# Kernel optimization log

Hardware: AMD Instinct MI355X
Metric: run time of the kernel (lower is better)

The kernel has to match this reference:

```python
import jax, jax.numpy as jnp
import numpy as np

N_NODE = 200000   # item catalog size (n_node)
EMB = 100         # emb_size
NNZ = 1000000     # hypergraph adjacency nonzeros
B = 1024          # batch / cl_size
L = 50            # session length
LAYERS = 2        # HyperConv layers (opt.layer)
TAU = 0.2         # contrastive temperature
K_NEI = 3         # FindNeighbors.neighbor_n


def setup_inputs() -> dict:
    key = jax.random.key(0)
    ks = jax.random.split(key, 16)
    g = 1.414 / np.sqrt(EMB)  # xavier_normal gain=1.414 scale
    inp = {}
    inp["embedding"] = jax.random.normal(ks[0], (N_NODE, EMB), jnp.float32) * 0.1
    inp["adj_val"] = jax.random.uniform(ks[1], (NNZ,), jnp.float32)
    inp["A"] = jax.random.uniform(ks[2], (B, B), jnp.float32) * 0.01
    inp["D"] = jax.random.uniform(ks[3], (B, B), jnp.float32) * 0.01
    inp["z2"] = jax.random.normal(ks[4], (B, EMB), jnp.float32)
    inp["Wcf1"] = jax.random.normal(ks[5], (EMB, EMB), jnp.float32) * g
    inp["bcf1"] = jnp.zeros((EMB,), jnp.float32)
    inp["Wcf2"] = jax.random.normal(ks[6], (EMB, EMB), jnp.float32) * g
    inp["bcf2"] = jnp.zeros((EMB,), jnp.float32)
    inp["Wkg1"] = jax.random.normal(ks[7], (EMB, EMB), jnp.float32) * g
    inp["bkg1"] = jnp.zeros((EMB,), jnp.float32)
    inp["Wkg2"] = jax.random.normal(ks[8], (EMB, EMB), jnp.float32) * g
    inp["bkg2"] = jnp.zeros((EMB,), jnp.float32)
    inp["session_len"] = jnp.full((B, 1), float(L), jnp.float32)
    inp["adj_row"] = jax.random.randint(ks[9], (NNZ,), 0, N_NODE, jnp.int32)
    inp["adj_col"] = jax.random.randint(ks[10], (NNZ,), 0, N_NODE, jnp.int32)
    inp["items"] = jax.random.randint(ks[11], (B, L), 0, N_NODE + 1, jnp.int32)
    return inp


def _proj(z, W1, b1, W2, b2):
    # nn.Linear -> ELU -> nn.Linear (Contrast_2view projector)
    return jax.nn.elu(z @ W1.T + b1) @ W2.T + b2


def reference(embedding, adj_val, A, D, z2,
              Wcf1, bcf1, Wcf2, bcf2, Wkg1, bkg1, Wkg2, bkg2,
              session_len, adj_row, adj_col, items):
    # ---- HyperConv: layered sparse propagation, averaged over layers ----
    h = embedding
    acc = embedding
    for _ in range(LAYERS):
        # torch.sparse.mm(adjacency, h) via gather + segment_sum
        h = jax.ops.segment_sum(adj_val[:, None] * h[adj_col], adj_row,
                                num_segments=N_NODE)
        acc = acc + h
    hyper = acc / (LAYERS + 1)  # [N_NODE, EMB]

    # ---- RelationGAT.forward ----
    emb_pad = jnp.concatenate([jnp.zeros((1, EMB), hyper.dtype), hyper], axis=0)
    seq_h = emb_pad[items]                       # [B, L, EMB]
    rel = jnp.sum(seq_h, axis=1) / session_len   # [B, EMB]
    rel = (D @ A) @ rel                          # session-graph conv
    c = jax.nn.selu(rel)
    l_c = c / jnp.linalg.norm(c, axis=-1, keepdims=True)  # [B, EMB]

    # ---- FindNeighbors (dropout omitted: eval mode) ----
    sess = l_c
    norms = jnp.sqrt(jnp.sum(sess * sess + 1e-6, axis=1, keepdims=True))
    cos = (sess @ sess.T) / (norms @ norms.T)    # [B, B]
    cos = jax.nn.softmax(cos, axis=-1)
    topv, topi = jax.lax.top_k(cos, K_NEI)       # [B, K]
    topv = jax.nn.softmax(topv, axis=-1)
    neighbor = jnp.sum(topv[:, :, None] * sess[topi], axis=1)  # [B, EMB]

    # ---- Contrast_2view ----
    z1p = _proj(sess, Wcf1, bcf1, Wcf2, bcf2)
    z2p = _proj(z2, Wkg1, bkg1, Wkg2, bkg2)
    n1 = jnp.linalg.norm(z1p, axis=-1, keepdims=True)
    n2 = jnp.linalg.norm(z2p, axis=-1, keepdims=True)
    simm = jnp.exp((z1p @ z2p.T) / (n1 @ n2.T) / TAU)
    simm = simm / (jnp.sum(simm, axis=1, keepdims=True) + 1e-8)
    cl_loss = -jnp.mean(jnp.log(jnp.diagonal(simm)))  # pos = eye

    return hyper, l_c, neighbor, cl_loss
```

## Files before the change

### kernel.cpp

```cpp
#include <hip/hip_runtime.h>
#include <hip/hip_bf16.h>

#define N_NODE 200000
#define EMB 100
#define NNZ 1000000
#define BATCH 1024
#define SLEN 50
#define BE (BATCH * EMB)
#define SCAN_BLK 1024
#define PROJ_ROWS 8
#define UNR 8
#define SPMM_BLOCKS 2048

#define OFF_LC    20000000LL
#define OFF_NB    20102400LL
#define OFF_LOSS  20204800LL

typedef __hip_bfloat16 bf16;

__device__ __forceinline__ float b2f(bf16 x) { return __bfloat162float(x); }
__device__ __forceinline__ bf16 f2b(float x) { return __float2bfloat16(x); }

__device__ __forceinline__ float ldf(const void* p, long long i, int f32) {
    return f32 ? ((const float*)p)[i] : b2f(((const bf16*)p)[i]);
}
__device__ __forceinline__ void stf(void* p, long long i, int f32, float v) {
    if (f32) ((float*)p)[i] = v;
    else     ((bf16*)p)[i] = f2b(v);
}

__device__ __forceinline__ float bfb2f(unsigned short s) {
    return __uint_as_float(((unsigned)s) << 16);
}
__device__ __forceinline__ unsigned short f2bfb(float x) {
    bf16 h = f2b(x); unsigned short r; __builtin_memcpy(&r, &h, 2); return r;
}
__device__ __forceinline__ float2 up2(unsigned u) {
    return make_float2(bfb2f((unsigned short)(u & 0xffff)), bfb2f((unsigned short)(u >> 16)));
}
__device__ __forceinline__ unsigned pk2(float a, float b) {
    return (unsigned)f2bfb(a) | ((unsigned)f2bfb(b) << 16);
}
__device__ __forceinline__ float2 ldf2(const void* p, long long pi, int f32) {
    if (f32) return ((const float2*)p)[pi];
    return up2(((const unsigned*)p)[pi]);
}
template<bool F32>
__device__ __forceinline__ float2 ldf2t(const void* p, long long pi) {
    if (F32) return ((const float2*)p)[pi];
    return up2(((const unsigned*)p)[pi]);
}
__device__ __forceinline__ void stf2(void* p, long long pi, int f32, float a, float b) {
    if (f32) ((float2*)p)[pi] = make_float2(a, b);
    else     ((unsigned*)p)[pi] = pk2(a, b);
}

__device__ __forceinline__ float wave_allreduce_sum(float v) {
    for (int m = 32; m > 0; m >>= 1) v += __shfl_xor(v, m, 64);
    return v;
}

__global__ void hist_kernel(const int* __restrict__ rows, int* __restrict__ counts,
                            const void* __restrict__ adjval, int* __restrict__ flag) {
    if (blockIdx.x == 0 && threadIdx.x == 0) {
        int f = 0;
        const bf16* p = (const bf16*)adjval;
        for (int i = 0; i < 64; i++) {
            float x = b2f(p[i]);
            if (!(x >= 0.0f && x <= 1.0f)) f = 1;
        }
        *flag = f;
    }
    int e = blockIdx.x * 256 + threadIdx.x;
    if (e < NNZ) atomicAdd(&counts[rows[e]], 1);
}

__global__ void scan_block(const int* __restrict__ counts, int* __restrict__ incl,
                           int* __restrict__ bsums) {
    __shared__ int s[SCAN_BLK];
    int i = blockIdx.x * SCAN_BLK + threadIdx.x;
    int v = (i < N_NODE) ? counts[i] : 0;
    s[threadIdx.x] = v;
    __syncthreads();
    for (int off = 1; off < SCAN_BLK; off <<= 1) {
        int add = (threadIdx.x >= (unsigned)off) ? s[threadIdx.x - off] : 0;
        __syncthreads();
        s[threadIdx.x] += add;
        __syncthreads();
    }
    if (i < N_NODE) incl[i] = s[threadIdx.x];
    if (threadIdx.x == SCAN_BLK - 1) bsums[blockIdx.x] = s[threadIdx.x];
}

__global__ void scan_top(int* __restrict__ bsums, int nb) {
    __shared__ int s[256];
    int t = threadIdx.x;
    int v = (t < nb) ? bsums[t] : 0;
    s[t] = v;
    __syncthreads();
    for (int off = 1; off < 256; off <<= 1) {
        int add = (t >= off) ? s[t - off] : 0;
        __syncthreads();
        s[t] += add;
        __syncthreads();
    }
    if (t < nb) bsums[t] = s[t] - v;
}

__global__ void scan_add(const int* __restrict__ counts, const int* __restrict__ incl,
                         const int* __restrict__ bsums, int* __restrict__ row_ptr,
                         int* __restrict__ cursor) {
    int i = blockIdx.x * SCAN_BLK + threadIdx.x;
    if (i < N_NODE) {
        int ex = incl[i] - counts[i] + bsums[blockIdx.x];
        row_ptr[i] = ex;
        cursor[i] = ex;
    }
    if (i == 0) row_ptr[N_NODE] = NNZ;
}

__global__ void permute_edges(const int* __restrict__ arow, const int* __restrict__ acol,
                              const void* __restrict__ aval, int* __restrict__ cursor,
                              int2* __restrict__ cv, const int* __restrict__ flagp) {
    const int f32 = *flagp;
    int e = blockIdx.x * 256 + threadIdx.x;
    if (e >= NNZ) return;
    int r = arow[e];
    int pos = atomicAdd(&cursor[r], 1);
    float v = ldf(aval, e, f32);
    cv[pos] = make_int2(acol[e], __float_as_int(v));
}

__device__ __forceinline__ void ld_batch_cv(int2* c, const int2* __restrict__ cv,
                                            int k0, int k1) {
    int ke = (k1 > k0) ? (k1 - 1) : 0;
    #pragma unroll
    for (int j = 0; j < UNR; j++) {
        int kk = k0 + j;
        c[j] = cv[kk < k1 ? kk : ke];
    }
}

template<bool F32>
__device__ __forceinline__ void spmm1_body(
        const int* __restrict__ rp, const int2* __restrict__ cv,
        const void* __restrict__ emb, unsigned* __restrict__ h1) {
    int nw = gridDim.x * 4;
    int wid = blockIdx.x * 4 + (threadIdx.x >> 6);
    int lane = threadIdx.x & 63;
    bool act = lane < 50;
    int pl = act ? lane : 0;

    int r = wid;
    if (r >= N_NODE) return;
    int k0 = rp[r], k1 = rp[r + 1];
    int2 cc[UNR];
    ld_batch_cv(cc, cv, k0, k1);
    int rn = r + nw;
    int k0n = 0, k1n = 0;
    if (rn < N_NODE) { k0n = rp[rn]; k1n = rp[rn + 1]; }

    for (;;) {
        float2 e[UNR];
        #pragma unroll
        for (int j = 0; j < UNR; j++)
            e[j] = ldf2t<F32>(emb, (long long)cc[j].x * 50 + pl);
        int2 cn[UNR];
        if (rn < N_NODE) ld_batch_cv(cn, cv, k0n, k1n);
        int rnn = rn + nw;
        int k0nn = 0, k1nn = 0;
        if (rnn < N_NODE) { k0nn = rp[rnn]; k1nn = rp[rnn + 1]; }

        float a0 = 0.f, a1 = 0.f;
        #pragma unroll
        for (int j = 0; j < UNR; j++) {
            float v = (k0 + j < k1) ? __int_as_float(cc[j].y) : 0.f;
            a0 += v * e[j].x; a1 += v * e[j].y;
        }
        for (int k = k0 + UNR; k < k1; k += UNR) {
            int2 ct[UNR];
            #pragma unroll
            for (int j = 0; j < UNR; j++) { int kk = k + j; ct[j] = cv[kk < k1 ? kk : k1 - 1]; }
            float2 et[UNR];
            #pragma unroll
            for (int j = 0; j < UNR; j++)
                et[j] = ldf2t<F32>(emb, (long long)ct[j].x * 50 + pl);
            #pragma unroll
            for (int j = 0; j < UNR; j++) {
                float v = (k + j < k1) ? __int_as_float(ct[j].y) : 0.f;
                a0 += v * et[j].x; a1 += v * et[j].y;
            }
        }
        if (act) h1[(long long)r * 50 + lane] = pk2(a0, a1);
        if (rn >= N_NODE) return;
        r = rn; k0 = k0n; k1 = k1n;
        #pragma unroll
        for (int j = 0; j < UNR; j++) cc[j] = cn[j];
        rn = rnn; k0n = k0nn; k1n = k1nn;
    }
}

__global__ __launch_bounds__(256) void spmm_gather1(
        const int* __restrict__ rp, const int2* __restrict__ cv,
        const void* __restrict__ emb,
        unsigned* __restrict__ h1, const int* __restrict__ flagp) {
    if (*flagp) spmm1_body<true>(rp, cv, emb, h1);
    else        spmm1_body<false>(rp, cv, emb, h1);
}

template<bool F32>
__device__ __forceinline__ void spmm2_body(
        const int* __restrict__ rp, const int2* __restrict__ cv,
        const void* __restrict__ emb,
        const unsigned* __restrict__ h1, void* __restrict__ out) {
    int nw = gridDim.x * 4;
    int wid = blockIdx.x * 4 + (threadIdx.x >> 6);
    int lane = threadIdx.x & 63;
    bool act = lane < 50;
    int pl = act ? lane : 0;

    int r = wid;
    if (r >= N_NODE) return;
    int k0 = rp[r], k1 = rp[r + 1];
    int2 cc[UNR];
    ld_batch_cv(cc, cv, k0, k1);
    int rn = r + nw;
    int k0n = 0, k1n = 0;
    if (rn < N_NODE) { k0n = rp[rn]; k1n = rp[rn + 1]; }

    for (;;) {
        float2 ebv = ldf2t<F32>(emb, (long long)r * 50 + pl);
        float2 h1r = up2(h1[(long long)r * 50 + pl]);
        float2 e[UNR];
        #pragma unroll
        for (int j = 0; j < UNR; j++)
            e[j] = up2(h1[(long long)cc[j].x * 50 + pl]);
        int2 cn[UNR];
        if (rn < N_NODE) ld_batch_cv(cn, cv, k0n, k1n);
        int rnn = rn + nw;
        int k0nn = 0, k1nn = 0;
        if (rnn < N_NODE) { k0nn = rp[rnn]; k1nn = rp[rnn + 1]; }

        float a0 = 0.f, a1 = 0.f;
        #pragma unroll
        for (int j = 0; j < UNR; j++) {
            float v = (k0 + j < k1) ? __int_as_float(cc[j].y) : 0.f;
            a0 += v * e[j].x; a1 += v * e[j].y;
        }
        for (int k = k0 + UNR; k < k1; k += UNR) {
            int2 ct[UNR];
            #pragma unroll
            for (int j = 0; j < UNR; j++) { int kk = k + j; ct[j] = cv[kk < k1 ? kk : k1 - 1]; }
            float2 et[UNR];
            #pragma unroll
            for (int j = 0; j < UNR; j++)
                et[j] = up2(h1[(long long)ct[j].x * 50 + pl]);
            #pragma unroll
            for (int j = 0; j < UNR; j++) {
                float v = (k + j < k1) ? __int_as_float(ct[j].y) : 0.f;
                a0 += v * et[j].x; a1 += v * et[j].y;
            }
        }
        if (act)
            stf2(out, (long long)r * 50 + lane, F32 ? 1 : 0,
                 (ebv.x + h1r.x + a0) * (1.0f / 3.0f), (ebv.y + h1r.y + a1) * (1.0f / 3.0f));
        if (rn >= N_NODE) return;
        r = rn; k0 = k0n; k1 = k1n;
        #pragma unroll
        for (int j = 0; j < UNR; j++) cc[j] = cn[j];
        rn = rnn; k0n = k0nn; k1n = k1nn;
    }
}

__global__ __launch_bounds__(256) void spmm_gather2(
        const int* __restrict__ rp, const int2* __restrict__ cv,
        const void* __restrict__ emb,
        const unsigned* __restrict__ h1, void* __restrict__ out,
        const int* __restrict__ flagp) {
    if (*flagp) spmm2_body<true>(rp, cv, emb, h1, out);
    else        spmm2_body<false>(rp, cv, emb, h1, out);
}

template<bool F32>
__device__ __forceinline__ void rel_rows_body(
        const void* __restrict__ out, const int* __restrict__ items,
        const void* __restrict__ slen, float* __restrict__ rel) {
    int lane = threadIdx.x & 63;
    int b = blockIdx.x * 4 + (threadIdx.x >> 6);
    if (b >= BATCH || lane >= 50) return;
    float s0 = 0.f, s1 = 0.f;
    #pragma unroll
    for (int l0 = 0; l0 < SLEN; l0 += 10) {
        int it[10];
        #pragma unroll
        for (int j = 0; j < 10; j++) it[j] = items[b * SLEN + l0 + j];
        float2 e[10];
        #pragma unroll
        for (int j = 0; j < 10; j++) {
            int idx = (it[j] > 0) ? it[j] - 1 : 0;
            e[j] = ldf2t<F32>(out, (long long)idx * 50 + lane);
        }
        #pragma unroll
        for (int j = 0; j < 10; j++) {
            float m = (it[j] > 0) ? 1.f : 0.f;
            s0 += m * e[j].x; s1 += m * e[j].y;
        }
    }
    float inv = 1.0f / ldf(slen, b, F32 ? 1 : 0);
    ((float2*)rel)[b * 50 + lane] = make_float2(s0 * inv, s1 * inv);
}

__global__ __launch_bounds__(256) void rel_rows(
        const void* __restrict__ out, const int* __restrict__ items,
        const void* __restrict__ slen, float* __restrict__ rel,
        const int* __restrict__ flagp) {
    if (*flagp) rel_rows_body<true>(out, items, slen, rel);
    else        rel_rows_body<false>(out, items, slen, rel);
}

template<int MODE>
__global__ __launch_bounds__(256) void bmm_rows_t(const void* __restrict__ M,
                                                  const float* __restrict__ X,
                                                  float* __restrict__ Y,
                                                  float* __restrict__ sess,
                                                  float* __restrict__ sessT,
                                                  float* __restrict__ ns,
                                                  void* __restrict__ out,
                                                  const int* __restrict__ flagp) {
    __shared__ float ms[4][BATCH];
    const int f32 = *flagp;
    int i0 = blockIdx.x * 4;
    int t = threadIdx.x;
    for (int idx = t; idx < 4 * BATCH; idx += 256) {
        int rr = idx >> 10, j = idx & 1023;
        ms[rr][j] = ldf(M, (long long)(i0 + rr) * BATCH + j, f32);
    }
    __syncthreads();
    int w = t >> 6, lane = t & 63;
    bool act = lane < 50;
    int i = i0 + w;
    float s0 = 0.f, s1 = 0.f;
    if (act) {
        const float2* X2 = (const float2*)X;
        for (int j = 0; j < BATCH; j++) {
            float m = ms[w][j];
            float2 x = X2[j * 50 + lane];
            s0 += m * x.x; s1 += m * x.y;
        }
    }
    if (MODE == 0) {
        if (act) ((float2*)Y)[i * 50 + lane] = make_float2(s0, s1);
        return;
    }
    const float sc = 1.0507009873554804934193349852946f;
    const float al = 1.6732632423543772848170429916717f;
    float c0 = (s0 > 0.f) ? sc * s0 : sc * (al * expm1f(s0));
    float c1 = (s1 > 0.f) ? sc * s1 : sc * (al * expm1f(s1));
    if (!act) { c0 = 0.f; c1 = 0.f; }
    float nrm = sqrtf(wave_allreduce_sum(c0 * c0 + c1 * c1));
    float l0 = c0 / nrm, l1 = c1 / nrm;
    float nterm = act ? (l0 * l0 + l1 * l1 + 2e-6f) : 0.f;
    float n2sum = wave_allreduce_sum(nterm);
    if (act) {
        ((float2*)sess)[i * 50 + lane] = make_float2(l0, l1);
        sessT[(2 * lane) * BATCH + i] = l0;
        sessT[(2 * lane + 1) * BATCH + i] = l1;
        stf2(out, OFF_LC / 2 + (long long)i * 50 + lane, f32, l0, l1);
    }
    if (lane == 0) ns[i] = sqrtf(n2sum);
}

__global__ void neighbor_kernel(const float* __restrict__ sess, const float* __restrict__ sessT,
                                const float* __restrict__ ns, void* __restrict__ out,
                                const int* __restrict__ flagp) {
    __shared__ float si[EMB];
    __shared__ float red[4];
    __shared__ float wrv[4]; __shared__ int wri[4];
    __shared__ float chv[3]; __shared__ int chi[3];
    __shared__ float stv[3];
    const int f32 = *flagp;
    int i = blockIdx.x, t = threadIdx.x;
    if (t < EMB) si[t] = sess[i * EMB + t];
    __syncthreads();
    float ni = ns[i];
    float d0 = 0.f, d1 = 0.f, d2 = 0.f, d3 = 0.f;
    for (int k = 0; k < EMB; k++) {
        float sv = si[k];
        const float* row = sessT + k * BATCH;
        d0 += sv * row[t];
        d1 += sv * row[t + 256];
        d2 += sv * row[t + 512];
        d3 += sv * row[t + 768];
    }
    float pv0 = expf(d0 / (ni * ns[t]));
    float pv1 = expf(d1 / (ni * ns[t + 256]));
    float pv2 = expf(d2 / (ni * ns[t + 512]));
    float pv3 = expf(d3 / (ni * ns[t + 768]));
    float local = pv0 + pv1 + pv2 + pv3;
    float w = wave_allreduce_sum(local);
    if ((t & 63) == 0) red[t >> 6] = w;
    __syncthreads();
    float S = red[0] + red[1] + red[2] + red[3];

    int c0 = -1, c1 = -1, c2 = -1;
    float pv[4] = {pv0, pv1, pv2, pv3};
    for (int r = 0; r < 3; r++) {
        float bv = -1e30f; int bi = 0x7fffffff;
        #pragma unroll
        for (int m = 0; m < 4; m++) {
            int j = t + (m << 8);
            if (j == c0 || j == c1 || j == c2) continue;
            float v = pv[m];
            if (v > bv || (v == bv && j < bi)) { bv = v; bi = j; }
        }
        #pragma unroll
        for (int off = 1; off < 64; off <<= 1) {
            float ov = __shfl_xor(bv, off);
            int oi = __shfl_xor(bi, off);
            if (ov > bv || (ov == bv && oi < bi)) { bv = ov; bi = oi; }
        }
        if ((t & 63) == 0) { wrv[t >> 6] = bv; wri[t >> 6] = bi; }
        __syncthreads();
        if (t == 0) {
            float fv = wrv[0]; int fi = wri[0];
            for (int wq = 1; wq < 4; wq++) {
                if (wrv[wq] > fv || (wrv[wq] == fv && wri[wq] < fi)) { fv = wrv[wq]; fi = wri[wq]; }
            }
            chv[r] = fv; chi[r] = fi;
        }
        __syncthreads();
        if (r == 0) c0 = chi[0];
        else if (r == 1) c1 = chi[1];
        else c2 = chi[2];
    }
    if (t == 0) {
        float e0 = expf(chv[0] / S), e1 = expf(chv[1] / S), e2 = expf(chv[2] / S);
        float es = e0 + e1 + e2;
        stv[0] = e0 / es; stv[1] = e1 / es; stv[2] = e2 / es;
    }
    __syncthreads();
    if (t < EMB) {
        float o = stv[0] * sess[chi[0] * EMB + t]
                + stv[1] * sess[chi[1] * EMB + t]
                + stv[2] * sess[chi[2] * EMB + t];
        stf(out, OFF_NB + i * EMB + t, f32, o);
    }
}

__global__ __launch_bounds__(256) void proj2(
        const void* __restrict__ X, int x_dual,
        const void* __restrict__ W1, const void* __restrict__ B1,
        const void* __restrict__ W2, const void* __restrict__ B2,
        float* __restrict__ Z, float* __restrict__ ZT, float* __restrict__ nrm,
        const int* __restrict__ flagp) {
    __shared__ float wT[EMB * EMB];
    __shared__ float bsh[EMB];
    __shared__ float hid[PROJ_ROWS][EMB];
    __shared__ float xr[2][EMB];
    __shared__ float red2[2][2];
    const int f32 = *flagp;
    int t = threadIdx.x;
    int sub = t >> 7, u = t & 127;
    int r0 = blockIdx.x * PROJ_ROWS;
    for (int idx = t; idx < EMB * EMB; idx += 256) {
        int o = idx / EMB, k = idx - o * EMB;
        wT[k * EMB + o] = ldf(W1, idx, f32);
    }
    if (t < EMB) bsh[t] = ldf(B1, t, f32);
    __syncthreads();
    for (int pr = 0; pr < PROJ_ROWS; pr += 2) {
        int row = r0 + pr + sub;
        if (u < EMB)
            xr[sub][u] = x_dual ? ldf(X, (long long)row * EMB + u, f32)
                                : ((const float*)X)[row * EMB + u];
        __syncthreads();
        if (u < EMB) {
            float s = bsh[u];
            for (int k = 0; k < EMB; k++) s += xr[sub][k] * wT[k * EMB + u];
            hid[pr + sub][u] = (s > 0.f) ? s : expm1f(s);
        }
        __syncthreads();
    }
    for (int idx = t; idx < EMB * EMB; idx += 256) {
        int o = idx / EMB, k = idx - o * EMB;
        wT[k * EMB + o] = ldf(W2, idx, f32);
    }
    if (t < EMB) bsh[t] = ldf(B2, t, f32);
    __syncthreads();
    for (int pr = 0; pr < PROJ_ROWS; pr += 2) {
        int row = r0 + pr + sub;
        float sq = 0.f;
        if (u < EMB) {
            float o = bsh[u];
            const float* h = hid[pr + sub];
            for (int k = 0; k < EMB; k++) o += h[k] * wT[k * EMB + u];
            Z[(long long)row * EMB + u] = o;
            if (ZT) ZT[(long long)u * BATCH + row] = o;
            sq = o * o;
        }
        sq = wave_allreduce_sum(sq);
        int w = t >> 6;
        if ((t & 63) == 0) red2[sub][w & 1] = sq;
        __syncthreads();
        if (u == 0) nrm[row] = sqrtf(red2[sub][0] + red2[sub][1]);
        __syncthreads();
    }
}

__global__ void loss_kernel(const float* __restrict__ z1p, const float* __restrict__ z2pT,
                            const float* __restrict__ n1, const float* __restrict__ n2,
                            float* __restrict__ acc) {
    __shared__ float zi[EMB];
    __shared__ float red[4];
    __shared__ float sdiag;
    int i = blockIdx.x, t = threadIdx.x;
    if (t < EMB) zi[t] = z1p[i * EMB + t];
    __syncthreads();
    float ni = n1[i];
    float d0 = 0.f, d1 = 0.f, d2 = 0.f, d3 = 0.f;
    for (int k = 0; k < EMB; k++) {
        float zv = zi[k];
        const float* row = z2pT + k * BATCH;
        d0 += zv * row[t];
        d1 += zv * row[t + 256];
        d2 += zv * row[t + 512];
        d3 += zv * row[t + 768];
    }
    float e0 = expf(d0 / (ni * n2[t]) * 5.0f);
    float e1 = expf(d1 / (ni * n2[t + 256]) * 5.0f);
    float e2 = expf(d2 / (ni * n2[t + 512]) * 5.0f);
    float e3 = expf(d3 / (ni * n2[t + 768]) * 5.0f);
    if (t == (i & 255)) {
        int m = i >> 8;
        sdiag = (m == 0) ? e0 : (m == 1) ? e1 : (m == 2) ? e2 : e3;
    }
    float local = e0 + e1 + e2 + e3;
    float w = wave_allreduce_sum(local);
    if ((t & 63) == 0) red[t >> 6] = w;
    __syncthreads();
    if (t == 0) {
        float S = red[0] + red[1] + red[2] + red[3];
        float l = -logf(sdiag / (S + 1e-8f));
        atomicAdd(acc, l * (1.0f / BATCH));
    }
}

__global__ void write_loss(const float* __restrict__ acc, void* __restrict__ out,
                           const int* __restrict__ flagp) {
    stf(out, OFF_LOSS, *flagp, acc[0]);
}

extern "C" void kernel_launch(void* const* d_in, const int* in_sizes, int n_in,
                              void* d_out, int out_size, void* d_ws, size_t ws_size,
                              hipStream_t stream) {
    const void* emb  = d_in[0];
    const void* aval = d_in[1];
    const void* Amat = d_in[2];
    const void* Dmat = d_in[3];
    const void* z2   = d_in[4];
    const void* Wcf1 = d_in[5];
    const void* bcf1 = d_in[6];
    const void* Wcf2 = d_in[7];
    const void* bcf2 = d_in[8];
    const void* Wkg1 = d_in[9];
    const void* bkg1 = d_in[10];
    const void* Wkg2 = d_in[11];
    const void* bkg2 = d_in[12];
    const void* slen = d_in[13];
    const int* arow  = (const int*)d_in[14];
    const int* acol  = (const int*)d_in[15];
    const int* items = (const int*)d_in[16];

    int* flag      = (int*)d_ws;
    int* counts    = (int*)((char*)d_ws + 256);
    int* cursor    = counts;
    int* row_ptr   = counts + N_NODE;
    int* bsums     = row_ptr + N_NODE + 64;
    int2* cv       = (int2*)(bsums + 256);
    int* scanbuf   = (int*)cv;
    unsigned* h1buf = (unsigned*)(cv + NNZ);
    float* fsmall  = (float*)(h1buf + (long long)N_NODE * 50);
    float* rel   = fsmall;
    float* t1    = rel  + BE;
    float* sess  = t1   + BE;
    float* sessT = sess + BE;
    float* z1p   = sessT + BE;
    float* z2p   = z1p  + BE;
    float* z2pT  = z2p  + BE;
    float* ns    = z2pT + BE;
    float* n1    = ns + BATCH;
    float* n2    = n1 + BATCH;
    float* lacc  = n2 + BATCH;

    const int nscan = (N_NODE + SCAN_BLK - 1) / SCAN_BLK;

    hipMemsetAsync(counts, 0, (size_t)N_NODE * sizeof(int), stream);
    hist_kernel<<<(NNZ + 255) / 256, 256, 0, stream>>>(arow, counts, aval, flag);
    scan_block<<<nscan, SCAN_BLK, 0, stream>>>(counts, scanbuf, bsums);
    scan_top<<<1, 256, 0, stream>>>(bsums, nscan);
    scan_add<<<nscan, SCAN_BLK, 0, stream>>>(counts, scanbuf, bsums, row_ptr, cursor);
    permute_edges<<<(NNZ + 255) / 256, 256, 0, stream>>>(arow, acol, aval, cursor,
                                                         cv, flag);

    spmm_gather1<<<SPMM_BLOCKS, 256, 0, stream>>>(row_ptr, cv, emb, h1buf, flag);
    spmm_gather2<<<SPMM_BLOCKS, 256, 0, stream>>>(row_ptr, cv, emb, h1buf,
                                                  d_out, flag);

    rel_rows<<<(BATCH + 3) / 4, 256, 0, stream>>>(d_out, items, slen, rel, flag);
    bmm_rows_t<0><<<BATCH / 4, 256, 0, stream>>>(Amat, rel, t1,
                                                 nullptr, nullptr, nullptr, nullptr, flag);
    bmm_rows_t<1><<<BATCH / 4, 256, 0, stream>>>(Dmat, t1, nullptr,
                                                 sess, sessT, ns, d_out, flag);

    neighbor_kernel<<<BATCH, 256, 0, stream>>>(sess, sessT, ns, d_out, flag);

    proj2<<<BATCH / PROJ_ROWS, 256, 0, stream>>>(sess, 0, Wcf1, bcf1, Wcf2, bcf2,
                                                 z1p, nullptr, n1, flag);
    proj2<<<BATCH / PROJ_ROWS, 256, 0, stream>>>(z2, 1, Wkg1, bkg1, Wkg2, bkg2,
                                                 z2p, z2pT, n2, flag);
    hipMemsetAsync(lacc, 0, sizeof(float), stream);
    loss_kernel<<<BATCH, 256, 0, stream>>>(z1p, z2pT, n1, n2, lacc);
    write_loss<<<1, 1, 0, stream>>>(lacc, d_out, flag);
}
```

Baseline: 740.7 us.

## Pad embeddings to 64-wide rows, fuse small kernels, simplify SpMM to one row per wave

Copies the embedding into a 64-wide padded layout so each wave's gathers fill a full row, and pads the h1 buffer the same way. The two SpMM kernels change from a persistent, software-pipelined grid-stride loop to a plain grid with one row per wave. Several launches are merged: the top-level scan is folded into scan_add, the z2 projection runs inside the first session matmul kernel, and the loss write-out moves into loss_kernel through a last-block counter. This adds an extra copy pass over the embedding and gives up the cross-row prefetch in the SpMM in exchange for fewer launches and aligned gathers.

Result: faster. 711.5 us (-3.9%).

```diff
diff --git a/kernel.cpp b/kernel.cpp
--- a/kernel.cpp
+++ b/kernel.cpp
@@ -10,7 +10,6 @@
 #define SCAN_BLK 1024
 #define PROJ_ROWS 8
 #define UNR 8
-#define SPMM_BLOCKS 2048
 
 #define OFF_LC    20000000LL
 #define OFF_NB    20102400LL
@@ -92,27 +91,24 @@
     if (threadIdx.x == SCAN_BLK - 1) bsums[blockIdx.x] = s[threadIdx.x];
 }
 
-__global__ void scan_top(int* __restrict__ bsums, int nb) {
+__global__ void scan_add(const int* __restrict__ counts, const int* __restrict__ incl,
+                         const int* __restrict__ bsums, int* __restrict__ row_ptr,
+                         int* __restrict__ cursor, int nb) {
     __shared__ int s[256];
     int t = threadIdx.x;
-    int v = (t < nb) ? bsums[t] : 0;
-    s[t] = v;
+    if (t < 256) s[t] = (t < nb) ? bsums[t] : 0;
     __syncthreads();
     for (int off = 1; off < 256; off <<= 1) {
-        int add = (t >= off) ? s[t - off] : 0;
-        __syncthreads();
-        s[t] += add;
-        __syncthreads();
-    }
-    if (t < nb) bsums[t] = s[t] - v;
-}
-
-__global__ void scan_add(const int* __restrict__ counts, const int* __restrict__ incl,
-                         const int* __restrict__ bsums, int* __restrict__ row_ptr,
-                         int* __restrict__ cursor) {
-    int i = blockIdx.x * SCAN_BLK + threadIdx.x;
+        int add = 0;
+        if (t < 256 && t >= off) add = s[t - off];
+        __syncthreads();
+        if (t < 256) s[t] += add;
+        __syncthreads();
+    }
+    int base = (blockIdx.x == 0) ? 0 : s[blockIdx.x - 1];
+    int i = blockIdx.x * SCAN_BLK + t;
     if (i < N_NODE) {
-        int ex = incl[i] - counts[i] + bsums[blockIdx.x];
+        int ex = incl[i] - counts[i] + base;
         row_ptr[i] = ex;
         cursor[i] = ex;
     }
@@ -124,6 +120,7 @@
                               int2* __restrict__ cv, const int* __restrict__ flagp) {
     const int f32 = *flagp;
     int e = blockIdx.x * 256 + threadIdx.x;
+    if (blockIdx.x == 0 && threadIdx.x < 8) cv[NNZ + threadIdx.x] = make_int2(0, 0);
     if (e >= NNZ) return;
     int r = arow[e];
     int pos = atomicAdd(&cursor[r], 1);
@@ -131,81 +128,70 @@
     cv[pos] = make_int2(acol[e], __float_as_int(v));
 }
 
-__device__ __forceinline__ void ld_batch_cv(int2* c, const int2* __restrict__ cv,
-                                            int k0, int k1) {
-    int ke = (k1 > k0) ? (k1 - 1) : 0;
+__global__ __launch_bounds__(256) void repack_emb(const void* __restrict__ emb,
+                                                  void* __restrict__ embp, int f32) {
+    long long idx = (long long)blockIdx.x * 256 + threadIdx.x;
+    if (idx >= (long long)N_NODE * 64) return;
+    long long r = idx >> 6;
+    int l = (int)(idx & 63);
+    float2 v = make_float2(0.f, 0.f);
+    if (l < 50) v = ldf2(emb, r * 50 + l, f32);
+    stf2(embp, r * 64 + l, f32, v.x, v.y);
+}
+
+__device__ __forceinline__ void ld_cv8(int2* c, const int2* __restrict__ cv, int k0) {
     #pragma unroll
-    for (int j = 0; j < UNR; j++) {
-        int kk = k0 + j;
-        c[j] = cv[kk < k1 ? kk : ke];
-    }
+    for (int j = 0; j < UNR; j++) c[j] = cv[k0 + j];
 }
 
 template<bool F32>
 __device__ __forceinline__ void spmm1_body(
         const int* __restrict__ rp, const int2* __restrict__ cv,
-        const void* __restrict__ emb, unsigned* __restrict__ h1) {
-    int nw = gridDim.x * 4;
-    int wid = blockIdx.x * 4 + (threadIdx.x >> 6);
+        const void* __restrict__ src, int estride, unsigned* __restrict__ h1) {
     int lane = threadIdx.x & 63;
+    int r = blockIdx.x * 4 + (threadIdx.x >> 6);
+    if (r >= N_NODE) return;
     bool act = lane < 50;
-    int pl = act ? lane : 0;
-
-    int r = wid;
-    if (r >= N_NODE) return;
+    int pl = (estride == 64) ? lane : (act ? lane : 0);
     int k0 = rp[r], k1 = rp[r + 1];
-    int2 cc[UNR];
-    ld_batch_cv(cc, cv, k0, k1);
-    int rn = r + nw;
-    int k0n = 0, k1n = 0;
-    if (rn < N_NODE) { k0n = rp[rn]; k1n = rp[rn + 1]; }
-
-    for (;;) {
-        float2 e[UNR];
+    int2 c[UNR];
+    ld_cv8(c, cv, k0);
+    int c0x = c[0].x;
+    float2 e[UNR];
+    #pragma unroll
+    for (int j = 0; j < UNR; j++) {
+        int cl = (k0 + j < k1) ? c[j].x : c0x;
+        e[j] = ldf2t<F32>(src, (long long)cl * estride + pl);
+    }
+    float a0 = 0.f, a1 = 0.f;
+    #pragma unroll
+    for (int j = 0; j < UNR; j++) {
+        float v = (k0 + j < k1) ? __int_as_float(c[j].y) : 0.f;
+        a0 += v * e[j].x; a1 += v * e[j].y;
+    }
+    for (int k = k0 + UNR; k < k1; k += UNR) {
+        int2 ct[UNR];
+        #pragma unroll
+        for (int j = 0; j < UNR; j++) { int kk = k + j; ct[j] = cv[kk < k1 ? kk : k1 - 1]; }
+        float2 et[UNR];
         #pragma unroll
         for (int j = 0; j < UNR; j++)
-            e[j] = ldf2t<F32>(emb, (long long)cc[j].x * 50 + pl);
-        int2 cn[UNR];
-        if (rn < N_NODE) ld_batch_cv(cn, cv, k0n, k1n);
-        int rnn = rn + nw;
-        int k0nn = 0, k1nn = 0;
-        if (rnn < N_NODE) { k0nn = rp[rnn]; k1nn = rp[rnn + 1]; }
-
-        float a0 = 0.f, a1 = 0.f;
+            et[j] = ldf2t<F32>(src, (long long)ct[j].x * estride + pl);
         #pragma unroll
         for (int j = 0; j < UNR; j++) {
-            float v = (k0 + j < k1) ? __int_as_float(cc[j].y) : 0.f;
-            a0 += v * e[j].x; a1 += v * e[j].y;
-        }
-        for (int k = k0 + UNR; k < k1; k += UNR) {
-            int2 ct[UNR];
-            #pragma unroll
-            for (int j = 0; j < UNR; j++) { int kk = k + j; ct[j] = cv[kk < k1 ? kk : k1 - 1]; }
-            float2 et[UNR];
-            #pragma unroll
-            for (int j = 0; j < UNR; j++)
-                et[j] = ldf2t<F32>(emb, (long long)ct[j].x * 50 + pl);
-            #pragma unroll
-            for (int j = 0; j < UNR; j++) {
-                float v = (k + j < k1) ? __int_as_float(ct[j].y) : 0.f;
-                a0 += v * et[j].x; a1 += v * et[j].y;
-            }
-        }
-        if (act) h1[(long long)r * 50 + lane] = pk2(a0, a1);
-        if (rn >= N_NODE) return;
-        r = rn; k0 = k0n; k1 = k1n;
-        #pragma unroll
-        for (int j = 0; j < UNR; j++) cc[j] = cn[j];
-        rn = rnn; k0n = k0nn; k1n = k1nn;
-    }
+            float v = (k + j < k1) ? __int_as_float(ct[j].y) : 0.f;
+            a0 += v * et[j].x; a1 += v * et[j].y;
+        }
+    }
+    h1[(long long)r * 64 + lane] = pk2(a0, a1);
 }
 
 __global__ __launch_bounds__(256) void spmm_gather1(
         const int* __restrict__ rp, const int2* __restrict__ cv,
-        const void* __restrict__ emb,
+        const void* __restrict__ src, int estride,
         unsigned* __restrict__ h1, const int* __restrict__ flagp) {
-    if (*flagp) spmm1_body<true>(rp, cv, emb, h1);
-    else        spmm1_body<false>(rp, cv, emb, h1);
+    if (*flagp) spmm1_body<true>(rp, cv, src, estride, h1);
+    else        spmm1_body<false>(rp, cv, src, estride, h1);
 }
 
 template<bool F32>
@@ -213,63 +199,46 @@
         const int* __restrict__ rp, const int2* __restrict__ cv,
         const void* __restrict__ emb,
         const unsigned* __restrict__ h1, void* __restrict__ out) {
-    int nw = gridDim.x * 4;
-    int wid = blockIdx.x * 4 + (threadIdx.x >> 6);
     int lane = threadIdx.x & 63;
+    int r = blockIdx.x * 4 + (threadIdx.x >> 6);
+    if (r >= N_NODE) return;
     bool act = lane < 50;
     int pl = act ? lane : 0;
-
-    int r = wid;
-    if (r >= N_NODE) return;
     int k0 = rp[r], k1 = rp[r + 1];
-    int2 cc[UNR];
-    ld_batch_cv(cc, cv, k0, k1);
-    int rn = r + nw;
-    int k0n = 0, k1n = 0;
-    if (rn < N_NODE) { k0n = rp[rn]; k1n = rp[rn + 1]; }
-
-    for (;;) {
-        float2 ebv = ldf2t<F32>(emb, (long long)r * 50 + pl);
-        float2 h1r = up2(h1[(long long)r * 50 + pl]);
-        float2 e[UNR];
+    int2 c[UNR];
+    ld_cv8(c, cv, k0);
+    int c0x = c[0].x;
+    float2 ebv = ldf2t<F32>(emb, (long long)r * 50 + pl);
+    float2 h1r = up2(h1[(long long)r * 64 + lane]);
+    float2 e[UNR];
+    #pragma unroll
+    for (int j = 0; j < UNR; j++) {
+        int cl = (k0 + j < k1) ? c[j].x : c0x;
+        e[j] = up2(h1[(long long)cl * 64 + lane]);
+    }
+    float a0 = 0.f, a1 = 0.f;
+    #pragma unroll
+    for (int j = 0; j < UNR; j++) {
+        float v = (k0 + j < k1) ? __int_as_float(c[j].y) : 0.f;
+        a0 += v * e[j].x; a1 += v * e[j].y;
+    }
+    for (int k = k0 + UNR; k < k1; k += UNR) {
+        int2 ct[UNR];
+        #pragma unroll
+        for (int j = 0; j < UNR; j++) { int kk = k + j; ct[j] = cv[kk < k1 ? kk : k1 - 1]; }
+        float2 et[UNR];
         #pragma unroll
         for (int j = 0; j < UNR; j++)
-            e[j] = up2(h1[(long long)cc[j].x * 50 + pl]);
-        int2 cn[UNR];
-        if (rn < N_NODE) ld_batch_cv(cn, cv, k0n, k1n);
-        int rnn = rn + nw;
-        int k0nn = 0, k1nn = 0;
-        if (rnn < N_NODE) { k0nn = rp[rnn]; k1nn = rp[rnn + 1]; }
-
-        float a0 = 0.f, a1 = 0.f;
+            et[j] = up2(h1[(long long)ct[j].x * 64 + lane]);
         #pragma unroll
         for (int j = 0; j < UNR; j++) {
-            float v = (k0 + j < k1) ? __int_as_float(cc[j].y) : 0.f;
-            a0 += v * e[j].x; a1 += v * e[j].y;
-        }
-        for (int k = k0 + UNR; k < k1; k += UNR) {
-            int2 ct[UNR];
-            #pragma unroll
-            for (int j = 0; j < UNR; j++) { int kk = k + j; ct[j] = cv[kk < k1 ? kk : k1 - 1]; }
-            float2 et[UNR];
-            #pragma unroll
-            for (int j = 0; j < UNR; j++)
-                et[j] = up2(h1[(long long)ct[j].x * 50 + pl]);
-            #pragma unroll
-            for (int j = 0; j < UNR; j++) {
-                float v = (k + j < k1) ? __int_as_float(ct[j].y) : 0.f;
-                a0 += v * et[j].x; a1 += v * et[j].y;
-            }
-        }
-        if (act)
-            stf2(out, (long long)r * 50 + lane, F32 ? 1 : 0,
-                 (ebv.x + h1r.x + a0) * (1.0f / 3.0f), (ebv.y + h1r.y + a1) * (1.0f / 3.0f));
-        if (rn >= N_NODE) return;
-        r = rn; k0 = k0n; k1 = k1n;
-        #pragma unroll
-        for (int j = 0; j < UNR; j++) cc[j] = cn[j];
-        rn = rnn; k0n = k0nn; k1n = k1nn;
-    }
+            float v = (k + j < k1) ? __int_as_float(ct[j].y) : 0.f;
+            a0 += v * et[j].x; a1 += v * et[j].y;
+        }
+    }
+    if (act)
+        stf2(out, (long long)r * 50 + lane, F32 ? 1 : 0,
+             (ebv.x + h1r.x + a0) * (1.0f / 3.0f), (ebv.y + h1r.y + a1) * (1.0f / 3.0f));
 }
 
 __global__ __launch_bounds__(256) void spmm_gather2(
@@ -318,17 +287,112 @@
     else        rel_rows_body<false>(out, items, slen, rel);
 }
 
-template<int MODE>
-__global__ __launch_bounds__(256) void bmm_rows_t(const void* __restrict__ M,
-                                                  const float* __restrict__ X,
-                                                  float* __restrict__ Y,
-                                                  float* __restrict__ sess,
-                                                  float* __restrict__ sessT,
-                                                  float* __restrict__ ns,
-                                                  void* __restrict__ out,
-                                                  const int* __restrict__ flagp) {
+__device__ __forceinline__ void bmm0_dev(float* smem, const void* __restrict__ M,
+                                         const float* __restrict__ X, float* __restrict__ Y,
+                                         int f32, int blk) {
+    float (*ms)[BATCH] = (float(*)[BATCH])smem;
+    int i0 = blk * 4;
+    int t = threadIdx.x;
+    for (int idx = t; idx < 4 * BATCH; idx += 256) {
+        int rr = idx >> 10, j = idx & 1023;
+        ms[rr][j] = ldf(M, (long long)(i0 + rr) * BATCH + j, f32);
+    }
+    __syncthreads();
+    int w = t >> 6, lane = t & 63;
+    if (lane >= 50) return;
+    int i = i0 + w;
+    const float2* X2 = (const float2*)X;
+    float s0 = 0.f, s1 = 0.f;
+    for (int j = 0; j < BATCH; j++) {
+        float m = ms[w][j];
+        float2 x = X2[j * 50 + lane];
+        s0 += m * x.x; s1 += m * x.y;
+    }
+    ((float2*)Y)[i * 50 + lane] = make_float2(s0, s1);
+}
+
+__device__ void proj_dev(float* smem, const void* __restrict__ X, int x_dual,
+                         const void* __restrict__ W1, const void* __restrict__ B1,
+                         const void* __restrict__ W2, const void* __restrict__ B2,
+                         float* __restrict__ Z, float* __restrict__ ZT,
+                         float* __restrict__ nrm, int f32, int blk) {
+    float* wT = smem;
+    float* bsh = smem + 10000;
+    float (*hid)[EMB] = (float(*)[EMB])(smem + 10100);
+    float (*xr)[EMB]  = (float(*)[EMB])(smem + 10900);
+    float (*red2)[2]  = (float(*)[2])(smem + 11100);
+    int t = threadIdx.x;
+    int sub = t >> 7, u = t & 127;
+    int r0 = blk * PROJ_ROWS;
+    for (int idx = t; idx < EMB * EMB; idx += 256) {
+        int o = idx / EMB, k = idx - o * EMB;
+        wT[k * EMB + o] = ldf(W1, idx, f32);
+    }
+    if (t < EMB) bsh[t] = ldf(B1, t, f32);
+    __syncthreads();
+    for (int pr = 0; pr < PROJ_ROWS; pr += 2) {
+        int row = r0 + pr + sub;
+        if (u < EMB)
+            xr[sub][u] = x_dual ? ldf(X, (long long)row * EMB + u, f32)
+                                : ((const float*)X)[row * EMB + u];
+        __syncthreads();
+        if (u < EMB) {
+            float s = bsh[u];
+            for (int k = 0; k < EMB; k++) s += xr[sub][k] * wT[k * EMB + u];
+            hid[pr + sub][u] = (s > 0.f) ? s : expm1f(s);
+        }
+        __syncthreads();
+    }
+    for (int idx = t; idx < EMB * EMB; idx += 256) {
+        int o = idx / EMB, k = idx - o * EMB;
+        wT[k * EMB + o] = ldf(W2, idx, f32);
+    }
+    if (t < EMB) bsh[t] = ldf(B2, t, f32);
+    __syncthreads();
+    for (int pr = 0; pr < PROJ_ROWS; pr += 2) {
+        int row = r0 + pr + sub;
+        float sq = 0.f;
+        if (u < EMB) {
+            float o = bsh[u];
+            const float* h = hid[pr + sub];
+            for (int k = 0; k < EMB; k++) o += h[k] * wT[k * EMB + u];
+            Z[(long long)row * EMB + u] = o;
+            if (ZT) ZT[(long long)u * BATCH + row] = o;
+            sq = o * o;
+        }
+        sq = wave_allreduce_sum(sq);
+        if ((t & 63) == 0) red2[sub][(t >> 6) & 1] = sq;
+        __syncthreads();
+        if (u == 0) nrm[row] = sqrtf(red2[sub][0] + red2[sub][1]);
+        __syncthreads();
+    }
+}
+
+__global__ __launch_bounds__(256) void bmm1_projz2(
+        const void* __restrict__ A, const float* __restrict__ relv, float* __restrict__ t1,
+        const void* __restrict__ z2,
+        const void* __restrict__ W1, const void* __restrict__ B1,
+        const void* __restrict__ W2, const void* __restrict__ B2,
+        float* __restrict__ z2p, float* __restrict__ z2pT, float* __restrict__ n2,
+        const int* __restrict__ flagp) {
+    __shared__ float smem[11104];
+    const int f32 = *flagp;
+    if (blockIdx.x < 256) bmm0_dev(smem, A, relv, t1, f32, blockIdx.x);
+    else proj_dev(smem, z2, 1, W1, B1, W2, B2, z2p, z2pT, n2, f32, blockIdx.x - 256);
+}
+
+__global__ __launch_bounds__(256) void bmm2_selu(const void* __restrict__ M,
+                                                 const float* __restrict__ X,
+                                                 float* __restrict__ sess,
+                                                 float* __restrict__ sessT,
+                                                 float* __restrict__ ns,
+                                                 void* __restrict__ out,
+                                                 float* __restrict__ lacc,
+                                                 int* __restrict__ done,
+                                                 const int* __restrict__ flagp) {
     __shared__ float ms[4][BATCH];
     const int f32 = *flagp;
+    if (blockIdx.x == 0 && threadIdx.x == 0) { *lacc = 0.f; *done = 0; }
     int i0 = blockIdx.x * 4;
     int t = threadIdx.x;
     for (int idx = t; idx < 4 * BATCH; idx += 256) {
@@ -347,10 +411,6 @@
             float2 x = X2[j * 50 + lane];
             s0 += m * x.x; s1 += m * x.y;
         }
-    }
-    if (MODE == 0) {
-        if (act) ((float2*)Y)[i * 50 + lane] = make_float2(s0, s1);
-        return;
     }
     const float sc = 1.0507009873554804934193349852946f;
     const float al = 1.6732632423543772848170429916717f;
@@ -447,72 +507,24 @@
     }
 }
 
-__global__ __launch_bounds__(256) void proj2(
-        const void* __restrict__ X, int x_dual,
+__global__ __launch_bounds__(256) void proj_z1(
+        const void* __restrict__ X,
         const void* __restrict__ W1, const void* __restrict__ B1,
         const void* __restrict__ W2, const void* __restrict__ B2,
-        float* __restrict__ Z, float* __restrict__ ZT, float* __restrict__ nrm,
+        float* __restrict__ Z, float* __restrict__ nrm,
         const int* __restrict__ flagp) {
-    __shared__ float wT[EMB * EMB];
-    __shared__ float bsh[EMB];
-    __shared__ float hid[PROJ_ROWS][EMB];
-    __shared__ float xr[2][EMB];
-    __shared__ float red2[2][2];
-    const int f32 = *flagp;
-    int t = threadIdx.x;
-    int sub = t >> 7, u = t & 127;
-    int r0 = blockIdx.x * PROJ_ROWS;
-    for (int idx = t; idx < EMB * EMB; idx += 256) {
-        int o = idx / EMB, k = idx - o * EMB;
-        wT[k * EMB + o] = ldf(W1, idx, f32);
-    }
-    if (t < EMB) bsh[t] = ldf(B1, t, f32);
-    __syncthreads();
-    for (int pr = 0; pr < PROJ_ROWS; pr += 2) {
-        int row = r0 + pr + sub;
-        if (u < EMB)
-            xr[sub][u] = x_dual ? ldf(X, (long long)row * EMB + u, f32)
-                                : ((const float*)X)[row * EMB + u];
-        __syncthreads();
-        if (u < EMB) {
-            float s = bsh[u];
-            for (int k = 0; k < EMB; k++) s += xr[sub][k] * wT[k * EMB + u];
-            hid[pr + sub][u] = (s > 0.f) ? s : expm1f(s);
-        }
-        __syncthreads();
-    }
-    for (int idx = t; idx < EMB * EMB; idx += 256) {
-        int o = idx / EMB, k = idx - o * EMB;
-        wT[k * EMB + o] = ldf(W2, idx, f32);
-    }
-    if (t < EMB) bsh[t] = ldf(B2, t, f32);
-    __syncthreads();
-    for (int pr = 0; pr < PROJ_ROWS; pr += 2) {
-        int row = r0 + pr + sub;
-        float sq = 0.f;
-        if (u < EMB) {
-            float o = bsh[u];
-            const float* h = hid[pr + sub];
-            for (int k = 0; k < EMB; k++) o += h[k] * wT[k * EMB + u];
-            Z[(long long)row * EMB + u] = o;
-            if (ZT) ZT[(long long)u * BATCH + row] = o;
-            sq = o * o;
-        }
-        sq = wave_allreduce_sum(sq);
-        int w = t >> 6;
-        if ((t & 63) == 0) red2[sub][w & 1] = sq;
-        __syncthreads();
-        if (u == 0) nrm[row] = sqrtf(red2[sub][0] + red2[sub][1]);
-        __syncthreads();
-    }
+    __shared__ float smem[11104];
+    proj_dev(smem, X, 0, W1, B1, W2, B2, Z, nullptr, nrm, *flagp, blockIdx.x);
 }
 
 __global__ void loss_kernel(const float* __restrict__ z1p, const float* __restrict__ z2pT,
                             const float* __restrict__ n1, const float* __restrict__ n2,
-                            float* __restrict__ acc) {
+                            float* __restrict__ acc, int* __restrict__ done,
+                            void* __restrict__ out, const int* __restrict__ flagp) {
     __shared__ float zi[EMB];
     __shared__ float red[4];
     __shared__ float sdiag;
+    const int f32 = *flagp;
     int i = blockIdx.x, t = threadIdx.x;
     if (t < EMB) zi[t] = z1p[i * EMB + t];
     __syncthreads();
@@ -542,12 +554,13 @@
         float S = red[0] + red[1] + red[2] + red[3];
         float l = -logf(sdiag / (S + 1e-8f));
         atomicAdd(acc, l * (1.0f / BATCH));
-    }
-}
-
-__global__ void write_loss(const float* __restrict__ acc, void* __restrict__ out,
-                           const int* __restrict__ flagp) {
-    stf(out, OFF_LOSS, *flagp, acc[0]);
+        __threadfence();
+        int old = atomicAdd(done, 1);
+        if (old == (int)gridDim.x - 1) {
+            float v = atomicAdd(acc, 0.0f);
+            stf(out, OFF_LOSS, f32, v);
+        }
+    }
 }
 
 extern "C" void kernel_launch(void* const* d_in, const int* in_sizes, int n_in,
@@ -571,6 +584,10 @@
     const int* acol  = (const int*)d_in[15];
     const int* items = (const int*)d_in[16];
 
+    long long esz = in_sizes ? (long long)in_sizes[0] : 0;
+    int f32_host = (esz == (long long)N_NODE * EMB * 4) ? 1 : 0;
+    int known_dtype = (esz == (long long)N_NODE * EMB * 2) || f32_host;
+
     int* flag      = (int*)d_ws;
     int* counts    = (int*)((char*)d_ws + 256);
     int* cursor    = counts;
@@ -578,8 +595,11 @@
     int* bsums     = row_ptr + N_NODE + 64;
     int2* cv       = (int2*)(bsums + 256);
     int* scanbuf   = (int*)cv;
-    unsigned* h1buf = (unsigned*)(cv + NNZ);
-    float* fsmall  = (float*)(h1buf + (long long)N_NODE * 50);
+    unsigned* h1buf = (unsigned*)(cv + NNZ + 8);
+    char* tailbase = (char*)(h1buf + (long long)N_NODE * 64);
+    void* emb_pad  = (void*)tailbase;
+    long long embpad_bytes = (long long)N_NODE * 64 * (f32_host ? 8 : 4);
+    float* fsmall  = (float*)tailbase;
     float* rel   = fsmall;
     float* t1    = rel  + BE;
     float* sess  = t1   + BE;
@@ -591,34 +611,44 @@
     float* n1    = ns + BATCH;
     float* n2    = n1 + BATCH;
     float* lacc  = n2 + BATCH;
+    int*   done  = (int*)(lacc + 1);
+    long long fsmall_bytes = ((char*)(done + 16)) - (char*)tailbase;
+    long long base_off = tailbase - (char*)d_ws;
+    long long need_pad = base_off + (embpad_bytes > fsmall_bytes ? embpad_bytes : fsmall_bytes);
+    int use_pad = known_dtype && ((long long)ws_size >= need_pad);
+    int estride = use_pad ? 64 : 50;
 
     const int nscan = (N_NODE + SCAN_BLK - 1) / SCAN_BLK;
 
     hipMemsetAsync(counts, 0, (size_t)N_NODE * sizeof(int), stream);
     hist_kernel<<<(NNZ + 255) / 256, 256, 0, stream>>>(arow, counts, aval, flag);
     scan_block<<<nscan, SCAN_BLK, 0, stream>>>(counts, scanbuf, bsums);
-    scan_top<<<1, 256, 0, stream>>>(bsums, nscan);
-    scan_add<<<nscan, SCAN_BLK, 0, stream>>>(counts, scanbuf, bsums, row_ptr, cursor);
+    scan_add<<<nscan, SCAN_BLK, 0, stream>>>(counts, scanbuf, bsums, row_ptr, cursor, nscan);
     permute_edges<<<(NNZ + 255) / 256, 256, 0, stream>>>(arow, acol, aval, cursor,
                                                          cv, flag);
 
-    spmm_gather1<<<SPMM_BLOCKS, 256, 0, stream>>>(row_ptr, cv, emb, h1buf, flag);
-    spmm_gather2<<<SPMM_BLOCKS, 256, 0, stream>>>(row_ptr, cv, emb, h1buf,
-                                                  d_out, flag);
+    if (use_pad) {
+        long long tot = (long long)N_NODE * 64;
+        repack_emb<<<(unsigned)((tot + 255) / 256), 256, 0, stream>>>(emb, emb_pad, f32_host);
+        spmm_gather1<<<(N_NODE + 3) / 4, 256, 0, stream>>>(row_ptr, cv, emb_pad, estride,
+                                                           h1buf, flag);
+    } else {
+        spmm_gather1<<<(N_NODE + 3) / 4, 256, 0, stream>>>(row_ptr, cv, emb, estride,
+                                                           h1buf, flag);
+    }
+    spmm_gather2<<<(N_NODE + 3) / 4, 256, 0, stream>>>(row_ptr, cv, emb, h1buf,
+                                                       d_out, flag);
 
     rel_rows<<<(BATCH + 3) / 4, 256, 0, stream>>>(d_out, items, slen, rel, flag);
-    bmm_rows_t<0><<<BATCH / 4, 256, 0, stream>>>(Amat, rel, t1,
-                                                 nullptr, nullptr, nullptr, nullptr, flag);
-    bmm_rows_t<1><<<BATCH / 4, 256, 0, stream>>>(Dmat, t1, nullptr,
-                                                 sess, sessT, ns, d_out, flag);
+    bmm1_projz2<<<384, 256, 0, stream>>>(Amat, rel, t1,
+                                         z2, Wkg1, bkg1, Wkg2, bkg2,
+                                         z2p, z2pT, n2, flag);
+    bmm2_selu<<<BATCH / 4, 256, 0, stream>>>(Dmat, t1, sess, sessT, ns, d_out,
+                                             lacc, done, flag);
 
     neighbor_kernel<<<BATCH, 256, 0, stream>>>(sess, sessT, ns, d_out, flag);
 
-    proj2<<<BATCH / PROJ_ROWS, 256, 0, stream>>>(sess, 0, Wcf1, bcf1, Wcf2, bcf2,
-                                                 z1p, nullptr, n1, flag);
-    proj2<<<BATCH / PROJ_ROWS, 256, 0, stream>>>(z2, 1, Wkg1, bkg1, Wkg2, bkg2,
-                                                 z2p, z2pT, n2, flag);
-    hipMemsetAsync(lacc, 0, sizeof(float), stream);
-    loss_kernel<<<BATCH, 256, 0, stream>>>(z1p, z2pT, n1, n2, lacc);
-    write_loss<<<1, 1, 0, stream>>>(lacc, d_out, flag);
-}
+    proj_z1<<<BATCH / PROJ_ROWS, 256, 0, stream>>>(sess, Wcf1, bcf1, Wcf2, bcf2,
+                                                   z1p, n1, flag);
+    loss_kernel<<<BATCH, 256, 0, stream>>>(z1p, z2pT, n1, n2, lacc, done, d_out, flag);
+}
```
